# Kernel optimization log

Measured on AMD Instinct MI355X. Metric: run time of the kernel, lower is better.

## Reference

```python
import jax, jax.numpy as jnp
import numpy as np

B, S, D = 4, 1568, 1024
H = 16
HD = D // H  # 64


def setup_inputs() -> dict:
    key = jax.random.key(0)
    ks = jax.random.split(key, 9)
    scale = 0.02
    return {
        "hidden_states": jax.random.normal(ks[0], (B, S, D), dtype=jnp.float32),
        "Wq": jax.random.normal(ks[1], (D, D), dtype=jnp.float32) * scale,
        "bq": jnp.zeros((D,), dtype=jnp.float32),
        "Wk": jax.random.normal(ks[2], (D, D), dtype=jnp.float32) * scale,
        "bk": jnp.zeros((D,), dtype=jnp.float32),
        "Wv": jax.random.normal(ks[3], (D, D), dtype=jnp.float32) * scale,
        "bv": jnp.zeros((D,), dtype=jnp.float32),
        "Wp": jax.random.normal(ks[4], (D, D), dtype=jnp.float32) * scale,
        "bp": jnp.zeros((D,), dtype=jnp.float32),
    }


def reference(hidden_states, Wq, bq, Wk, bk, Wv, bv, Wp, bp):
    x = hidden_states  # [B, S, D]
    # Linear projections (torch Linear: x @ W.T + b)
    q = x @ Wq.T + bq
    k = x @ Wk.T + bk
    v = x @ Wv.T + bv
    # split heads: [B, H, S, HD]
    def heads(t):
        return t.reshape(B, S, H, HD).transpose(0, 2, 1, 3)
    q, k, v = heads(q), heads(k), heads(v)
    scale = 1.0 / jnp.sqrt(jnp.asarray(HD, dtype=q.dtype))
    scores = jnp.einsum('bhqd,bhkd->bhqk', q, k) * scale  # [B,H,S,S]
    probs = jax.nn.softmax(scores, axis=-1)
    ctx = jnp.einsum('bhqk,bhkd->bhqd', probs, v)  # [B,H,S,HD]
    ctx = ctx.transpose(0, 2, 1, 3).reshape(B, S, D)
    out = ctx @ Wp.T + bp
    return out
```

## Files before the change

### kernel.cpp

```cpp
#include <hip/hip_runtime.h>
#include <stdint.h>

#define SEQ 1568
#define SEQV 1600
#define DIM 1024
#define NB 4
#define NH 16
#define HD 64

typedef unsigned short u16;
typedef __bf16 bf16x8 __attribute__((ext_vector_type(8)));
typedef __bf16 bf16x4 __attribute__((ext_vector_type(4)));
typedef float f32x4 __attribute__((ext_vector_type(4)));

#define QSCALE 0.18033688011112042f

#define PSTR 72

__device__ __forceinline__ void load_lds16(const u16* g, u16* s) {
  __builtin_amdgcn_global_load_lds((__attribute__((address_space(1))) void*)g,
                                   (__attribute__((address_space(3))) void*)s,
                                   16, 0, 0);
}

#define WAIT_VM(N) asm volatile("s_waitcnt vmcnt(" #N ")" ::: "memory")
#define LGKM0()    asm volatile("s_waitcnt lgkmcnt(0)" ::: "memory")
#define BAR()      do { __builtin_amdgcn_s_barrier(); \
                        __builtin_amdgcn_sched_barrier(0); } while (0)

__global__ __launch_bounds__(256) void cvt_all(
    const float* __restrict__ x,  const float* __restrict__ wq,
    const float* __restrict__ wk, const float* __restrict__ wv,
    const float* __restrict__ wp,
    u16* __restrict__ xb, u16* __restrict__ wqb, u16* __restrict__ wkb,
    u16* __restrict__ wvb, u16* __restrict__ wpb) {
  int i = blockIdx.x * 256 + threadIdx.x;
  const float* src; u16* dst; int off;
  if (i < 1605632)      { src = x;  dst = xb;  off = i; }
  else if (i < 1867776) { src = wq; dst = wqb; off = i - 1605632; }
  else if (i < 2129920) { src = wk; dst = wkb; off = i - 1867776; }
  else if (i < 2392064) { src = wv; dst = wvb; off = i - 2129920; }
  else                  { src = wp; dst = wpb; off = i - 2392064; }
  float4 v = ((const float4*)src)[off];
  union { unsigned long long u; __bf16 h[4]; } o;
  o.h[0] = (__bf16)v.x; o.h[1] = (__bf16)v.y;
  o.h[2] = (__bf16)v.z; o.h[3] = (__bf16)v.w;
  ((unsigned long long*)dst)[off] = o.u;
}

__global__ __launch_bounds__(256) void gemm_qkv(
    const u16* __restrict__ xb,
    const u16* __restrict__ wq, const u16* __restrict__ wk, const u16* __restrict__ wv,
    const float* __restrict__ bq, const float* __restrict__ bk, const float* __restrict__ bv,
    u16* __restrict__ qo, u16* __restrict__ ko, u16* __restrict__ vto) {
  const int bid = blockIdx.x;
  const int logical = (bid & 7) * 147 + (bid >> 3);
  const int z   = logical / 392;
  const int rem = logical % 392;
  const int bm  = (rem >> 3) * 128;
  const int bn  = (rem & 7) * 128;

  const u16* W = (z == 0) ? wq : (z == 1) ? wk : wv;
  const float* bias = (z == 0) ? bq : (z == 1) ? bk : bv;

  __shared__ __align__(16) u16 sA[3][128 * 32];
  __shared__ __align__(16) u16 sB[3][128 * 32];

  const int tid = threadIdx.x;
  const int wave = tid >> 6;
  const int lane = tid & 63;
  const int l15 = lane & 15;
  const int quad = lane >> 4;
  const int wm = (wave >> 1) * 64;
  const int wn = (wave & 1) * 64;

  const int sr  = lane >> 2;
  const int scs = (((lane & 3) ^ ((lane >> 3) & 3)) << 3);
  const int r0 = wave * 32;

  const u16* gA1 = xb + (size_t)(bm + r0 + sr) * DIM + scs;
  const u16* gA2 = gA1 + 16 * DIM;
  const u16* gB1 = W + (size_t)(bn + r0 + sr) * DIM + scs;
  const u16* gB2 = gB1 + 16 * DIM;

  f32x4 acc[4][4] = {};
  const int rsw = (l15 >> 1) & 3;

  auto stage = [&](int kk, u16* sAc, u16* sBc) {
    load_lds16(gA1 + kk, sAc + r0 * 32);
    load_lds16(gA2 + kk, sAc + (r0 + 16) * 32);
    load_lds16(gB1 + kk, sBc + r0 * 32);
    load_lds16(gB2 + kk, sBc + (r0 + 16) * 32);
  };

  auto mstep = [&](const u16* sAc, const u16* sBc) {
    bf16x8 a[4], b[4];
#pragma unroll
    for (int mt = 0; mt < 4; mt++)
      a[mt] = *(const bf16x8*)&sAc[(wm + mt * 16 + l15) * 32 + ((quad ^ rsw) << 3)];
#pragma unroll
    for (int nt = 0; nt < 4; nt++)
      b[nt] = *(const bf16x8*)&sBc[(wn + nt * 16 + l15) * 32 + ((quad ^ rsw) << 3)];
#pragma unroll
    for (int mt = 0; mt < 4; mt++)
#pragma unroll
      for (int nt = 0; nt < 4; nt++)
        acc[mt][nt] = __builtin_amdgcn_mfma_f32_16x16x32_bf16(a[mt], b[nt], acc[mt][nt], 0, 0, 0);
  };

  stage(0,  &sA[0][0], &sB[0][0]);
  stage(32, &sA[1][0], &sB[1][0]);
  stage(64, &sA[2][0], &sB[2][0]);

#pragma unroll 1
  for (int t = 0; t < 30; t += 3) {
    WAIT_VM(8); BAR();
    mstep(&sA[0][0], &sB[0][0]);
    LGKM0(); BAR();
    stage((t + 3) * 32, &sA[0][0], &sB[0][0]);

    WAIT_VM(8); BAR();
    mstep(&sA[1][0], &sB[1][0]);
    LGKM0(); BAR();
    stage((t + 4) * 32, &sA[1][0], &sB[1][0]);

    WAIT_VM(8); BAR();
    mstep(&sA[2][0], &sB[2][0]);
    LGKM0(); BAR();
    if (t + 5 < 32) stage((t + 5) * 32, &sA[2][0], &sB[2][0]);
  }
  WAIT_VM(4); BAR();
  mstep(&sA[0][0], &sB[0][0]);
  WAIT_VM(0); BAR();
  mstep(&sA[1][0], &sB[1][0]);

#pragma unroll
  for (int nt = 0; nt < 4; nt++) {
    const int n = bn + wn + nt * 16 + l15;
    const float bia = bias[n];
    const int h = n >> 6, d = n & 63;
#pragma unroll
    for (int mt = 0; mt < 4; mt++) {
      const int rbase = bm + wm + mt * 16 + quad * 4;
#pragma unroll
      for (int r = 0; r < 4; r++) {
        const int row = rbase + r;
        const int bi = row / SEQ;
        const int s  = row - bi * SEQ;
        float val = acc[mt][nt][r] + bia;
        if (z == 0) val *= QSCALE;
        const __bf16 o = (__bf16)val;
        if (z == 0)
          *(__bf16*)&qo[(((size_t)(bi * NH + h)) * SEQ + s) * HD + d] = o;
        else if (z == 1)
          *(__bf16*)&ko[(((size_t)(bi * NH + h)) * SEQ + s) * HD + d] = o;
        else
          *(__bf16*)&vto[(((size_t)(bi * NH + h)) * HD + d) * SEQV + s] = o;
      }
    }
  }
}

__global__ __launch_bounds__(256, 4) void attn(
    const u16* __restrict__ q, const u16* __restrict__ k,
    const u16* __restrict__ vt, u16* __restrict__ ctx) {
  const int bid = blockIdx.x;
  const int logical = (bid & 7) * 104 + (bid >> 3);
  const int bh = logical / 13;
  const int qt = logical % 13;
  const int tid = threadIdx.x;
  const int wave = tid >> 6, lane = tid & 63, l15 = lane & 15, quad = lane >> 4;

  __shared__ __align__(16) u16 sK[64 * 64];
  __shared__ __align__(16) u16 sV[64 * 64];
  __shared__ __align__(16) u16 sP[4][32 * PSTR];

  const u16* qh = q + (size_t)bh * (SEQ * HD);
  const u16* kh = k + (size_t)bh * (SEQ * HD);
  const u16* vh = vt + (size_t)bh * (HD * SEQV);

  bf16x8 aq[2][2];
#pragma unroll
  for (int mt = 0; mt < 2; mt++) {
    int qrow = qt * 128 + wave * 32 + mt * 16 + l15;
    int qr = qrow < SEQ ? qrow : SEQ - 1;
    aq[mt][0] = *(const bf16x8*)&qh[(size_t)qr * HD + quad * 8];
    aq[mt][1] = *(const bf16x8*)&qh[(size_t)qr * HD + 32 + quad * 8];
  }

  f32x4 o[2][4] = {};
  float lsum[2] = {0.0f, 0.0f};

  const int jrow = lane >> 3;
  const int cg = (lane & 7) ^ jrow;
  u16* sPw = sP[wave];
  const int j7 = l15 & 7;

  for (int j0 = 0; j0 < 1536; j0 += 64) {
    __syncthreads();
    load_lds16(&kh[(size_t)(j0 + wave * 16 + jrow) * HD + cg * 8], &sK[(wave * 16) * 64]);
    load_lds16(&kh[(size_t)(j0 + wave * 16 + 8 + jrow) * HD + cg * 8], &sK[(wave * 16 + 8) * 64]);
    load_lds16(&vh[(size_t)(wave * 16 + jrow) * SEQV + j0 + cg * 8], &sV[(wave * 16) * 64]);
    load_lds16(&vh[(size_t)(wave * 16 + 8 + jrow) * SEQV + j0 + cg * 8], &sV[(wave * 16 + 8) * 64]);
    __syncthreads();

#pragma unroll
    for (int mt = 0; mt < 2; mt++) {
      f32x4 s[4];
      __builtin_amdgcn_s_setprio(1);
#pragma unroll
      for (int jt = 0; jt < 4; jt++) {
        const int j = jt * 16 + l15;
        bf16x8 b0 = *(const bf16x8*)&sK[j * 64 + ((quad ^ j7) * 8)];
        bf16x8 b1 = *(const bf16x8*)&sK[j * 64 + (((4 + quad) ^ j7) * 8)];
        f32x4 acc = {};
        acc = __builtin_amdgcn_mfma_f32_16x16x32_bf16(b0, aq[mt][0], acc, 0, 0, 0);
        acc = __builtin_amdgcn_mfma_f32_16x16x32_bf16(b1, aq[mt][1], acc, 0, 0, 0);
        s[jt] = acc;
      }
      __builtin_amdgcn_s_setprio(0);
#pragma unroll
      for (int jt = 0; jt < 4; jt++) {
        bf16x4 pk;
#pragma unroll
        for (int r = 0; r < 4; r++) {
          float p = __builtin_exp2f(s[jt][r]);
          lsum[mt] += p;
          pk[r] = (__bf16)p;
        }
        *(bf16x4*)&sPw[(mt * 16 + l15) * PSTR + jt * 16 + quad * 4] = pk;
      }
    }

    LGKM0();

    __builtin_amdgcn_s_setprio(1);
#pragma unroll
    for (int kc = 0; kc < 2; kc++) {
      bf16x8 ap0 = *(const bf16x8*)&sPw[l15 * PSTR + kc * 32 + quad * 8];
      bf16x8 ap1 = *(const bf16x8*)&sPw[(16 + l15) * PSTR + kc * 32 + quad * 8];
#pragma unroll
      for (int dt = 0; dt < 4; dt++) {
        const int d7 = l15 & 7;
        bf16x8 bv = *(const bf16x8*)&sV[(dt * 16 + l15) * 64 + (((kc * 4 + quad) ^ d7) * 8)];
        o[0][dt] = __builtin_amdgcn_mfma_f32_16x16x32_bf16(ap0, bv, o[0][dt], 0, 0, 0);
        o[1][dt] = __builtin_amdgcn_mfma_f32_16x16x32_bf16(ap1, bv, o[1][dt], 0, 0, 0);
      }
    }
    __builtin_amdgcn_s_setprio(0);
  }

  {
    const int j0 = 1536;
    __syncthreads();
    if (wave < 2) {
      load_lds16(&kh[(size_t)(j0 + wave * 16 + jrow) * HD + cg * 8], &sK[(wave * 16) * 64]);
      load_lds16(&kh[(size_t)(j0 + wave * 16 + 8 + jrow) * HD + cg * 8], &sK[(wave * 16 + 8) * 64]);
    }
    load_lds16(&vh[(size_t)(wave * 16 + jrow) * SEQV + j0 + cg * 8], &sV[(wave * 16) * 64]);
    load_lds16(&vh[(size_t)(wave * 16 + 8 + jrow) * SEQV + j0 + cg * 8], &sV[(wave * 16 + 8) * 64]);
    __syncthreads();

#pragma unroll
    for (int mt = 0; mt < 2; mt++) {
      f32x4 s[2];
#pragma unroll
      for (int jt = 0; jt < 2; jt++) {
        const int j = jt * 16 + l15;
        bf16x8 b0 = *(const bf16x8*)&sK[j * 64 + ((quad ^ j7) * 8)];
        bf16x8 b1 = *(const bf16x8*)&sK[j * 64 + (((4 + quad) ^ j7) * 8)];
        f32x4 acc = {};
        acc = __builtin_amdgcn_mfma_f32_16x16x32_bf16(b0, aq[mt][0], acc, 0, 0, 0);
        acc = __builtin_amdgcn_mfma_f32_16x16x32_bf16(b1, aq[mt][1], acc, 0, 0, 0);
        s[jt] = acc;
      }
#pragma unroll
      for (int jt = 0; jt < 2; jt++) {
        bf16x4 pk;
#pragma unroll
        for (int r = 0; r < 4; r++) {
          float p = __builtin_exp2f(s[jt][r]);
          lsum[mt] += p;
          pk[r] = (__bf16)p;
        }
        *(bf16x4*)&sPw[(mt * 16 + l15) * PSTR + jt * 16 + quad * 4] = pk;
      }
    }

    LGKM0();

    {
      bf16x8 ap0 = *(const bf16x8*)&sPw[l15 * PSTR + quad * 8];
      bf16x8 ap1 = *(const bf16x8*)&sPw[(16 + l15) * PSTR + quad * 8];
#pragma unroll
      for (int dt = 0; dt < 4; dt++) {
        const int d7 = l15 & 7;
        bf16x8 bv = *(const bf16x8*)&sV[(dt * 16 + l15) * 64 + ((quad ^ d7) * 8)];
        o[0][dt] = __builtin_amdgcn_mfma_f32_16x16x32_bf16(ap0, bv, o[0][dt], 0, 0, 0);
        o[1][dt] = __builtin_amdgcn_mfma_f32_16x16x32_bf16(ap1, bv, o[1][dt], 0, 0, 0);
      }
    }
  }

  const int bi = bh >> 4, h = bh & 15;
  float Lq[2][4];
#pragma unroll
  for (int mt = 0; mt < 2; mt++) {
    float l = lsum[mt];
    l += __shfl_xor(l, 16);
    l += __shfl_xor(l, 32);
#pragma unroll
    for (int r = 0; r < 4; r++)
      Lq[mt][r] = __shfl(l, quad * 4 + r, 16);
  }
#pragma unroll
  for (int mt = 0; mt < 2; mt++) {
#pragma unroll
    for (int r = 0; r < 4; r++) {
      const int srow = qt * 128 + wave * 32 + mt * 16 + quad * 4 + r;
      if (srow < SEQ) {
        const float inv = 1.0f / Lq[mt][r];
#pragma unroll
        for (int dt = 0; dt < 4; dt++)
          *(__bf16*)&ctx[((size_t)(bi * SEQ + srow)) * DIM + h * HD + dt * 16 + l15] =
              (__bf16)(o[mt][dt][r] * inv);
      }
    }
  }
}

__global__ __launch_bounds__(256) void gemm_out(
    const u16* __restrict__ ctx, const u16* __restrict__ wp,
    const float* __restrict__ bp, float* __restrict__ out) {
  const int bid = blockIdx.x;
  const int logical = (bid & 7) * 49 + (bid >> 3);
  const int bm = (logical >> 3) * 128;
  const int bn = (logical & 7) * 128;

  __shared__ __align__(16) u16 sA[3][128 * 32];
  __shared__ __align__(16) u16 sB[3][128 * 32];

  const int tid = threadIdx.x;
  const int wave = tid >> 6;
  const int lane = tid & 63;
  const int l15 = lane & 15;
  const int quad = lane >> 4;
  const int wm = (wave >> 1) * 64;
  const int wn = (wave & 1) * 64;
  const int sr  = lane >> 2;
  const int scs = (((lane & 3) ^ ((lane >> 3) & 3)) << 3);
  const int r0 = wave * 32;

  const u16* gA1 = ctx + (size_t)(bm + r0 + sr) * DIM + scs;
  const u16* gA2 = gA1 + 16 * DIM;
  const u16* gB1 = wp + (size_t)(bn + r0 + sr) * DIM + scs;
  const u16* gB2 = gB1 + 16 * DIM;

  f32x4 acc[4][4] = {};
  const int rsw = (l15 >> 1) & 3;

  auto stage = [&](int kk, u16* sAc, u16* sBc) {
    load_lds16(gA1 + kk, sAc + r0 * 32);
    load_lds16(gA2 + kk, sAc + (r0 + 16) * 32);
    load_lds16(gB1 + kk, sBc + r0 * 32);
    load_lds16(gB2 + kk, sBc + (r0 + 16) * 32);
  };

  auto mstep = [&](const u16* sAc, const u16* sBc) {
    bf16x8 a[4], b[4];
#pragma unroll
    for (int mt = 0; mt < 4; mt++)
      a[mt] = *(const bf16x8*)&sAc[(wm + mt * 16 + l15) * 32 + ((quad ^ rsw) << 3)];
#pragma unroll
    for (int nt = 0; nt < 4; nt++)
      b[nt] = *(const bf16x8*)&sBc[(wn + nt * 16 + l15) * 32 + ((quad ^ rsw) << 3)];
#pragma unroll
    for (int mt = 0; mt < 4; mt++)
#pragma unroll
      for (int nt = 0; nt < 4; nt++)
        acc[mt][nt] = __builtin_amdgcn_mfma_f32_16x16x32_bf16(a[mt], b[nt], acc[mt][nt], 0, 0, 0);
  };

  stage(0,  &sA[0][0], &sB[0][0]);
  stage(32, &sA[1][0], &sB[1][0]);
  stage(64, &sA[2][0], &sB[2][0]);

#pragma unroll 1
  for (int t = 0; t < 30; t += 3) {
    WAIT_VM(8); BAR();
    mstep(&sA[0][0], &sB[0][0]);
    LGKM0(); BAR();
    stage((t + 3) * 32, &sA[0][0], &sB[0][0]);

    WAIT_VM(8); BAR();
    mstep(&sA[1][0], &sB[1][0]);
    LGKM0(); BAR();
    stage((t + 4) * 32, &sA[1][0], &sB[1][0]);

    WAIT_VM(8); BAR();
    mstep(&sA[2][0], &sB[2][0]);
    LGKM0(); BAR();
    if (t + 5 < 32) stage((t + 5) * 32, &sA[2][0], &sB[2][0]);
  }
  WAIT_VM(4); BAR();
  mstep(&sA[0][0], &sB[0][0]);
  WAIT_VM(0); BAR();
  mstep(&sA[1][0], &sB[1][0]);

#pragma unroll
  for (int nt = 0; nt < 4; nt++) {
    const int n = bn + wn + nt * 16 + l15;
    const float bia = bp[n];
#pragma unroll
    for (int mt = 0; mt < 4; mt++) {
      const int mbase = bm + wm + mt * 16 + quad * 4;
#pragma unroll
      for (int r = 0; r < 4; r++)
        out[(size_t)(mbase + r) * DIM + n] = acc[mt][nt][r] + bia;
    }
  }
}

extern "C" void kernel_launch(void* const* d_in, const int* in_sizes, int n_in,
                              void* d_out, int out_size, void* d_ws, size_t ws_size,
                              hipStream_t stream) {
  const float* x  = (const float*)d_in[0];
  const float* Wq = (const float*)d_in[1];
  const float* bq = (const float*)d_in[2];
  const float* Wk = (const float*)d_in[3];
  const float* bk = (const float*)d_in[4];
  const float* Wv = (const float*)d_in[5];
  const float* bv = (const float*)d_in[6];
  const float* Wp = (const float*)d_in[7];
  const float* bp = (const float*)d_in[8];
  float* out = (float*)d_out;

  char* ws = (char*)d_ws;
  u16* xb   = (u16*)(ws + 0);
  u16* wqb  = (u16*)(ws + 12845056);
  u16* wkb  = (u16*)(ws + 14942208);
  u16* wvb  = (u16*)(ws + 17039360);
  u16* wpb  = (u16*)(ws + 19136512);
  u16* qb   = (u16*)(ws + 21233664);
  u16* kb   = (u16*)(ws + 34078720);
  u16* vtb  = (u16*)(ws + 46923776);
  u16* ctxb = (u16*)(ws + 60030976);

  cvt_all<<<10368, 256, 0, stream>>>(x, Wq, Wk, Wv, Wp, xb, wqb, wkb, wvb, wpb);
  gemm_qkv<<<1176, 256, 0, stream>>>(xb, wqb, wkb, wvb, bq, bk, bv, qb, kb, vtb);
  attn<<<832, 256, 0, stream>>>(qb, kb, vtb, ctxb);
  gemm_out<<<392, 256, 0, stream>>>(ctxb, wpb, bp, out);
}
```

Before: 292.9 us.

## Use 7-wave attention blocks covering 224 queries; tile QKV GEMM per batch

The attention kernel now launches 448 blocks of 7 waves, each covering 224 query rows, instead of 832 blocks of 4 waves covering 128. Since 1568 = 7*224, the padded last query tile and its bounds checks go away. Each K/V tile loaded into LDS is also reused by more waves. The QKV GEMM switches to a 3D grid tiled per batch with 13 sequence tiles per batch, clamping padded rows and masking their stores; this adds some wasted MMA work but removes the per-row divide. The launch bound drops the occupancy hint, which risks higher register pressure and fewer resident blocks.

```diff
diff --git a/kernel.cpp b/kernel.cpp
--- a/kernel.cpp
+++ b/kernel.cpp
@@ -53,12 +53,14 @@
     const u16* __restrict__ wq, const u16* __restrict__ wk, const u16* __restrict__ wv,
     const float* __restrict__ bq, const float* __restrict__ bk, const float* __restrict__ bv,
     u16* __restrict__ qo, u16* __restrict__ ko, u16* __restrict__ vto) {
-  const int bid = blockIdx.x;
-  const int logical = (bid & 7) * 147 + (bid >> 3);
-  const int z   = logical / 392;
-  const int rem = logical % 392;
-  const int bm  = (rem >> 3) * 128;
-  const int bn  = (rem & 7) * 128;
+  const int bid = blockIdx.x + (blockIdx.y << 3) + blockIdx.z * 416;
+  const int logical = (bid & 7) * 156 + (bid >> 3);
+  const int byz = logical >> 3;
+  const int by  = byz % 52;
+  const int z   = byz / 52;
+  const int bi  = by / 13;
+  const int st  = by % 13;
+  const int bn  = (logical & 7) * 128;
 
   const u16* W = (z == 0) ? wq : (z == 1) ? wk : wv;
   const float* bias = (z == 0) ? bq : (z == 1) ? bk : bv;
@@ -78,8 +80,10 @@
   const int scs = (((lane & 3) ^ ((lane >> 3) & 3)) << 3);
   const int r0 = wave * 32;
 
-  const u16* gA1 = xb + (size_t)(bm + r0 + sr) * DIM + scs;
-  const u16* gA2 = gA1 + 16 * DIM;
+  int ra1 = st * 128 + r0 + sr;       if (ra1 >= SEQ) ra1 = SEQ - 1;
+  int ra2 = st * 128 + r0 + 16 + sr;  if (ra2 >= SEQ) ra2 = SEQ - 1;
+  const u16* gA1 = xb + (size_t)(bi * SEQ + ra1) * DIM + scs;
+  const u16* gA2 = xb + (size_t)(bi * SEQ + ra2) * DIM + scs;
   const u16* gB1 = W + (size_t)(bn + r0 + sr) * DIM + scs;
   const u16* gB2 = gB1 + 16 * DIM;
 
@@ -141,39 +145,39 @@
     const int h = n >> 6, d = n & 63;
 #pragma unroll
     for (int mt = 0; mt < 4; mt++) {
-      const int rbase = bm + wm + mt * 16 + quad * 4;
+      const int sbase = st * 128 + wm + mt * 16 + quad * 4;
 #pragma unroll
       for (int r = 0; r < 4; r++) {
-        const int row = rbase + r;
-        const int bi = row / SEQ;
-        const int s  = row - bi * SEQ;
-        float val = acc[mt][nt][r] + bia;
-        if (z == 0) val *= QSCALE;
-        const __bf16 o = (__bf16)val;
-        if (z == 0)
-          *(__bf16*)&qo[(((size_t)(bi * NH + h)) * SEQ + s) * HD + d] = o;
-        else if (z == 1)
-          *(__bf16*)&ko[(((size_t)(bi * NH + h)) * SEQ + s) * HD + d] = o;
-        else
-          *(__bf16*)&vto[(((size_t)(bi * NH + h)) * HD + d) * SEQV + s] = o;
-      }
-    }
-  }
-}
-
-__global__ __launch_bounds__(256, 4) void attn(
+        const int s = sbase + r;
+        if (s < SEQ) {
+          float val = acc[mt][nt][r] + bia;
+          if (z == 0) val *= QSCALE;
+          const __bf16 o = (__bf16)val;
+          if (z == 0)
+            *(__bf16*)&qo[(((size_t)(bi * NH + h)) * SEQ + s) * HD + d] = o;
+          else if (z == 1)
+            *(__bf16*)&ko[(((size_t)(bi * NH + h)) * SEQ + s) * HD + d] = o;
+          else
+            *(__bf16*)&vto[(((size_t)(bi * NH + h)) * HD + d) * SEQV + s] = o;
+        }
+      }
+    }
+  }
+}
+
+__global__ __launch_bounds__(448) void attn(
     const u16* __restrict__ q, const u16* __restrict__ k,
     const u16* __restrict__ vt, u16* __restrict__ ctx) {
   const int bid = blockIdx.x;
-  const int logical = (bid & 7) * 104 + (bid >> 3);
-  const int bh = logical / 13;
-  const int qt = logical % 13;
+  const int logical = (bid & 7) * 56 + (bid >> 3);
+  const int bh = logical / 7;
+  const int qt = logical % 7;
   const int tid = threadIdx.x;
   const int wave = tid >> 6, lane = tid & 63, l15 = lane & 15, quad = lane >> 4;
 
   __shared__ __align__(16) u16 sK[64 * 64];
   __shared__ __align__(16) u16 sV[64 * 64];
-  __shared__ __align__(16) u16 sP[4][32 * PSTR];
+  __shared__ __align__(16) u16 sP[7][32 * PSTR];
 
   const u16* qh = q + (size_t)bh * (SEQ * HD);
   const u16* kh = k + (size_t)bh * (SEQ * HD);
@@ -182,10 +186,9 @@
   bf16x8 aq[2][2];
 #pragma unroll
   for (int mt = 0; mt < 2; mt++) {
-    int qrow = qt * 128 + wave * 32 + mt * 16 + l15;
-    int qr = qrow < SEQ ? qrow : SEQ - 1;
-    aq[mt][0] = *(const bf16x8*)&qh[(size_t)qr * HD + quad * 8];
-    aq[mt][1] = *(const bf16x8*)&qh[(size_t)qr * HD + 32 + quad * 8];
+    const int qrow = qt * 224 + wave * 32 + mt * 16 + l15;
+    aq[mt][0] = *(const bf16x8*)&qh[(size_t)qrow * HD + quad * 8];
+    aq[mt][1] = *(const bf16x8*)&qh[(size_t)qrow * HD + 32 + quad * 8];
   }
 
   f32x4 o[2][4] = {};
@@ -198,10 +201,15 @@
 
   for (int j0 = 0; j0 < 1536; j0 += 64) {
     __syncthreads();
-    load_lds16(&kh[(size_t)(j0 + wave * 16 + jrow) * HD + cg * 8], &sK[(wave * 16) * 64]);
-    load_lds16(&kh[(size_t)(j0 + wave * 16 + 8 + jrow) * HD + cg * 8], &sK[(wave * 16 + 8) * 64]);
-    load_lds16(&vh[(size_t)(wave * 16 + jrow) * SEQV + j0 + cg * 8], &sV[(wave * 16) * 64]);
-    load_lds16(&vh[(size_t)(wave * 16 + 8 + jrow) * SEQV + j0 + cg * 8], &sV[(wave * 16 + 8) * 64]);
+    if (wave < 4) {
+      load_lds16(&kh[(size_t)(j0 + wave * 16 + jrow) * HD + cg * 8], &sK[(wave * 16) * 64]);
+      load_lds16(&kh[(size_t)(j0 + wave * 16 + 8 + jrow) * HD + cg * 8], &sK[(wave * 16 + 8) * 64]);
+    }
+    if (wave >= 3) {
+      const int vw = wave - 3;
+      load_lds16(&vh[(size_t)(vw * 16 + jrow) * SEQV + j0 + cg * 8], &sV[(vw * 16) * 64]);
+      load_lds16(&vh[(size_t)(vw * 16 + 8 + jrow) * SEQV + j0 + cg * 8], &sV[(vw * 16 + 8) * 64]);
+    }
     __syncthreads();
 
 #pragma unroll
@@ -257,8 +265,11 @@
       load_lds16(&kh[(size_t)(j0 + wave * 16 + jrow) * HD + cg * 8], &sK[(wave * 16) * 64]);
       load_lds16(&kh[(size_t)(j0 + wave * 16 + 8 + jrow) * HD + cg * 8], &sK[(wave * 16 + 8) * 64]);
     }
-    load_lds16(&vh[(size_t)(wave * 16 + jrow) * SEQV + j0 + cg * 8], &sV[(wave * 16) * 64]);
-    load_lds16(&vh[(size_t)(wave * 16 + 8 + jrow) * SEQV + j0 + cg * 8], &sV[(wave * 16 + 8) * 64]);
+    if (wave >= 3) {
+      const int vw = wave - 3;
+      load_lds16(&vh[(size_t)(vw * 16 + jrow) * SEQV + j0 + cg * 8], &sV[(vw * 16) * 64]);
+      load_lds16(&vh[(size_t)(vw * 16 + 8 + jrow) * SEQV + j0 + cg * 8], &sV[(vw * 16 + 8) * 64]);
+    }
     __syncthreads();
 
 #pragma unroll
@@ -317,14 +328,12 @@
   for (int mt = 0; mt < 2; mt++) {
 #pragma unroll
     for (int r = 0; r < 4; r++) {
-      const int srow = qt * 128 + wave * 32 + mt * 16 + quad * 4 + r;
-      if (srow < SEQ) {
-        const float inv = 1.0f / Lq[mt][r];
-#pragma unroll
-        for (int dt = 0; dt < 4; dt++)
-          *(__bf16*)&ctx[((size_t)(bi * SEQ + srow)) * DIM + h * HD + dt * 16 + l15] =
-              (__bf16)(o[mt][dt][r] * inv);
-      }
+      const int srow = qt * 224 + wave * 32 + mt * 16 + quad * 4 + r;
+      const float inv = 1.0f / Lq[mt][r];
+#pragma unroll
+      for (int dt = 0; dt < 4; dt++)
+        *(__bf16*)&ctx[((size_t)(bi * SEQ + srow)) * DIM + h * HD + dt * 16 + l15] =
+            (__bf16)(o[mt][dt][r] * inv);
     }
   }
 }
@@ -447,7 +456,7 @@
   u16* ctxb = (u16*)(ws + 60030976);
 
   cvt_all<<<10368, 256, 0, stream>>>(x, Wq, Wk, Wv, Wp, xb, wqb, wkb, wvb, wpb);
-  gemm_qkv<<<1176, 256, 0, stream>>>(xb, wqb, wkb, wvb, bq, bk, bv, qb, kb, vtb);
-  attn<<<832, 256, 0, stream>>>(qb, kb, vtb, ctxb);
+  gemm_qkv<<<dim3(8, 52, 3), 256, 0, stream>>>(xb, wqb, wkb, wvb, bq, bk, bv, qb, kb, vtb);
+  attn<<<448, 448, 0, stream>>>(qb, kb, vtb, ctxb);
   gemm_out<<<392, 256, 0, stream>>>(ctxb, wpb, bp, out);
 }
```

New measurement: 306.9 us. 1.05x slower.

## Compute softmax row sums via MFMA with ones and tile QKV GEMM per batch

Applied to the files above, without the earlier changes.

The attention kernel drops the per-element scalar accumulation of exp values and the cross-lane shuffles at the end. Instead it computes row sums with an extra MFMA against a vector of bf16 ones, reusing the P fragments already loaded. This removes VALU adds from the softmax inner loop at the cost of two more MFMAs per chunk and summing bf16-rounded probabilities. The QKV GEMM grid becomes per-batch 128-row tiles (13 per batch, padded with clamped rows) so each tile's batch index is fixed, which removes per-element divisions in the epilogue but adds some padded wasted work.

```diff
diff --git a/kernel.cpp b/kernel.cpp
--- a/kernel.cpp
+++ b/kernel.cpp
@@ -53,12 +53,14 @@
     const u16* __restrict__ wq, const u16* __restrict__ wk, const u16* __restrict__ wv,
     const float* __restrict__ bq, const float* __restrict__ bk, const float* __restrict__ bv,
     u16* __restrict__ qo, u16* __restrict__ ko, u16* __restrict__ vto) {
-  const int bid = blockIdx.x;
-  const int logical = (bid & 7) * 147 + (bid >> 3);
-  const int z   = logical / 392;
-  const int rem = logical % 392;
-  const int bm  = (rem >> 3) * 128;
-  const int bn  = (rem & 7) * 128;
+  const int bid = blockIdx.x + (blockIdx.y << 3) + blockIdx.z * 416;
+  const int logical = (bid & 7) * 156 + (bid >> 3);
+  const int byz = logical >> 3;
+  const int by  = byz % 52;
+  const int z   = byz / 52;
+  const int bi  = by / 13;
+  const int st  = by % 13;
+  const int bn  = (logical & 7) * 128;
 
   const u16* W = (z == 0) ? wq : (z == 1) ? wk : wv;
   const float* bias = (z == 0) ? bq : (z == 1) ? bk : bv;
@@ -78,8 +80,10 @@
   const int scs = (((lane & 3) ^ ((lane >> 3) & 3)) << 3);
   const int r0 = wave * 32;
 
-  const u16* gA1 = xb + (size_t)(bm + r0 + sr) * DIM + scs;
-  const u16* gA2 = gA1 + 16 * DIM;
+  int ra1 = st * 128 + r0 + sr;       if (ra1 >= SEQ) ra1 = SEQ - 1;
+  int ra2 = st * 128 + r0 + 16 + sr;  if (ra2 >= SEQ) ra2 = SEQ - 1;
+  const u16* gA1 = xb + (size_t)(bi * SEQ + ra1) * DIM + scs;
+  const u16* gA2 = xb + (size_t)(bi * SEQ + ra2) * DIM + scs;
   const u16* gB1 = W + (size_t)(bn + r0 + sr) * DIM + scs;
   const u16* gB2 = gB1 + 16 * DIM;
 
@@ -141,21 +145,21 @@
     const int h = n >> 6, d = n & 63;
 #pragma unroll
     for (int mt = 0; mt < 4; mt++) {
-      const int rbase = bm + wm + mt * 16 + quad * 4;
+      const int sbase = st * 128 + wm + mt * 16 + quad * 4;
 #pragma unroll
       for (int r = 0; r < 4; r++) {
-        const int row = rbase + r;
-        const int bi = row / SEQ;
-        const int s  = row - bi * SEQ;
-        float val = acc[mt][nt][r] + bia;
-        if (z == 0) val *= QSCALE;
-        const __bf16 o = (__bf16)val;
-        if (z == 0)
-          *(__bf16*)&qo[(((size_t)(bi * NH + h)) * SEQ + s) * HD + d] = o;
-        else if (z == 1)
-          *(__bf16*)&ko[(((size_t)(bi * NH + h)) * SEQ + s) * HD + d] = o;
-        else
-          *(__bf16*)&vto[(((size_t)(bi * NH + h)) * HD + d) * SEQV + s] = o;
+        const int s = sbase + r;
+        if (s < SEQ) {
+          float val = acc[mt][nt][r] + bia;
+          if (z == 0) val *= QSCALE;
+          const __bf16 o = (__bf16)val;
+          if (z == 0)
+            *(__bf16*)&qo[(((size_t)(bi * NH + h)) * SEQ + s) * HD + d] = o;
+          else if (z == 1)
+            *(__bf16*)&ko[(((size_t)(bi * NH + h)) * SEQ + s) * HD + d] = o;
+          else
+            *(__bf16*)&vto[(((size_t)(bi * NH + h)) * HD + d) * SEQV + s] = o;
+        }
       }
     }
   }
@@ -188,8 +192,11 @@
     aq[mt][1] = *(const bf16x8*)&qh[(size_t)qr * HD + 32 + quad * 8];
   }
 
+  const __bf16 kOne = (__bf16)1.0f;
+  const bf16x8 vone = {kOne, kOne, kOne, kOne, kOne, kOne, kOne, kOne};
+
   f32x4 o[2][4] = {};
-  float lsum[2] = {0.0f, 0.0f};
+  f32x4 ol[2] = {};
 
   const int jrow = lane >> 3;
   const int cg = (lane & 7) ^ jrow;
@@ -223,11 +230,8 @@
       for (int jt = 0; jt < 4; jt++) {
         bf16x4 pk;
 #pragma unroll
-        for (int r = 0; r < 4; r++) {
-          float p = __builtin_exp2f(s[jt][r]);
-          lsum[mt] += p;
-          pk[r] = (__bf16)p;
-        }
+        for (int r = 0; r < 4; r++)
+          pk[r] = (__bf16)__builtin_exp2f(s[jt][r]);
         *(bf16x4*)&sPw[(mt * 16 + l15) * PSTR + jt * 16 + quad * 4] = pk;
       }
     }
@@ -246,6 +250,8 @@
         o[0][dt] = __builtin_amdgcn_mfma_f32_16x16x32_bf16(ap0, bv, o[0][dt], 0, 0, 0);
         o[1][dt] = __builtin_amdgcn_mfma_f32_16x16x32_bf16(ap1, bv, o[1][dt], 0, 0, 0);
       }
+      ol[0] = __builtin_amdgcn_mfma_f32_16x16x32_bf16(ap0, vone, ol[0], 0, 0, 0);
+      ol[1] = __builtin_amdgcn_mfma_f32_16x16x32_bf16(ap1, vone, ol[1], 0, 0, 0);
     }
     __builtin_amdgcn_s_setprio(0);
   }
@@ -278,11 +284,8 @@
       for (int jt = 0; jt < 2; jt++) {
         bf16x4 pk;
 #pragma unroll
-        for (int r = 0; r < 4; r++) {
-          float p = __builtin_exp2f(s[jt][r]);
-          lsum[mt] += p;
-          pk[r] = (__bf16)p;
-        }
+        for (int r = 0; r < 4; r++)
+          pk[r] = (__bf16)__builtin_exp2f(s[jt][r]);
         *(bf16x4*)&sPw[(mt * 16 + l15) * PSTR + jt * 16 + quad * 4] = pk;
       }
     }
@@ -299,27 +302,19 @@
         o[0][dt] = __builtin_amdgcn_mfma_f32_16x16x32_bf16(ap0, bv, o[0][dt], 0, 0, 0);
         o[1][dt] = __builtin_amdgcn_mfma_f32_16x16x32_bf16(ap1, bv, o[1][dt], 0, 0, 0);
       }
+      ol[0] = __builtin_amdgcn_mfma_f32_16x16x32_bf16(ap0, vone, ol[0], 0, 0, 0);
+      ol[1] = __builtin_amdgcn_mfma_f32_16x16x32_bf16(ap1, vone, ol[1], 0, 0, 0);
     }
   }
 
   const int bi = bh >> 4, h = bh & 15;
-  float Lq[2][4];
-#pragma unroll
-  for (int mt = 0; mt < 2; mt++) {
-    float l = lsum[mt];
-    l += __shfl_xor(l, 16);
-    l += __shfl_xor(l, 32);
-#pragma unroll
-    for (int r = 0; r < 4; r++)
-      Lq[mt][r] = __shfl(l, quad * 4 + r, 16);
-  }
 #pragma unroll
   for (int mt = 0; mt < 2; mt++) {
 #pragma unroll
     for (int r = 0; r < 4; r++) {
       const int srow = qt * 128 + wave * 32 + mt * 16 + quad * 4 + r;
       if (srow < SEQ) {
-        const float inv = 1.0f / Lq[mt][r];
+        const float inv = 1.0f / ol[mt][r];
 #pragma unroll
         for (int dt = 0; dt < 4; dt++)
           *(__bf16*)&ctx[((size_t)(bi * SEQ + srow)) * DIM + h * HD + dt * 16 + l15] =
@@ -447,7 +442,7 @@
   u16* ctxb = (u16*)(ws + 60030976);
 
   cvt_all<<<10368, 256, 0, stream>>>(x, Wq, Wk, Wv, Wp, xb, wqb, wkb, wvb, wpb);
-  gemm_qkv<<<1176, 256, 0, stream>>>(xb, wqb, wkb, wvb, bq, bk, bv, qb, kb, vtb);
+  gemm_qkv<<<dim3(8, 52, 3), 256, 0, stream>>>(xb, wqb, wkb, wvb, bq, bk, bv, qb, kb, vtb);
   attn<<<832, 256, 0, stream>>>(qb, kb, vtb, ctxb);
   gemm_out<<<392, 256, 0, stream>>>(ctxb, wpb, bp, out);
 }
```

Result: faster. 281.2 us, median of 2 (-4.0%).
